# Optimization experiments

Measured on AMD Instinct MI355X. Metric: run time of the kernel, lower is better.

## Reference

```python
import jax, jax.numpy as jnp
import numpy as np

B, N, D, L = 8, 2048, 1024, 128


def setup_inputs() -> dict:
    key = jax.random.key(0)
    ks = jax.random.split(key, 8)
    return {
        "e_i_t_minus_1": jax.random.normal(ks[0], (B, D), dtype=jnp.float32),
        "e_j_t": jax.random.normal(ks[1], (B, N, D), dtype=jnp.float32),
        "imp_j_t": jax.random.uniform(ks[2], (B, N), dtype=jnp.float32),
        "R_lk": jax.random.normal(ks[3], (L, D), dtype=jnp.float32),
        "W_q": jax.random.normal(ks[4], (D, D), dtype=jnp.float32) * (D ** -0.5),
        "W_k": jax.random.normal(ks[5], (D, D), dtype=jnp.float32) * (D ** -0.5),
        "W_v": jax.random.normal(ks[6], (D, D), dtype=jnp.float32) * (D ** -0.5),
        "omega": jax.random.normal(ks[7], (D,), dtype=jnp.float32),
    }


def reference(e_i_t_minus_1, e_j_t, imp_j_t, R_lk, W_q, W_k, W_v, omega):
    # torch nn.Linear(x) = x @ W.T  (weights stored [out, in])
    q_i = jnp.einsum('bd,ed->be', e_i_t_minus_1, W_q)[:, None, :]   # [B,1,D]
    k_j = jnp.einsum('bnd,ed->bne', e_j_t, W_k)                      # [B,N,D]
    sigma = jnp.einsum('bnd,d->bn', jnp.tanh(q_i + k_j), omega)      # [B,N]
    exp_sigma = jnp.exp(sigma)
    sum_exp = jnp.sum(exp_sigma, axis=1, keepdims=True)              # [B,1]
    a_ij = imp_j_t * exp_sigma / (sum_exp + 1e-9)                    # [B,N]
    v_j = jnp.einsum('bnd,ed->bne', e_j_t, W_v)                      # [B,N,D]
    A = jnp.einsum('bn,bnd->bd', a_ij, v_j)                          # [B,D]
    # R_lk[l,d] * a_ij[b,n] * v_j[b,n,d], summed over n -> [B,L,D]
    A_lk = jnp.einsum('bn,bnd,ld->bld', a_ij, v_j, R_lk)             # [B,L,D]
    A_l = A                                                          # identical math in source
    return (A, A_lk, A_l)
```

## Files before the change

kernel.cpp:

```cpp
#include <hip/hip_runtime.h>
#include <hip/hip_bf16.h>
#include <math.h>

#define BB 8
#define NN 2048
#define DD 1024
#define LL 128
#define MM (BB*NN)

typedef _Float16 half8 __attribute__((ext_vector_type(8)));
typedef _Float16 half4 __attribute__((ext_vector_type(4)));
typedef __attribute__((ext_vector_type(4))) float floatx4;

__device__ __forceinline__ void glds16(const void* g, void* l) {
    __builtin_amdgcn_global_load_lds(
        (const __attribute__((address_space(1))) unsigned int*)g,
        (__attribute__((address_space(3))) unsigned int*)l, 16, 0, 0);
}

__global__ __launch_bounds__(256) void prep_kernel(const float* __restrict__ e_j,
                                                   _Float16* __restrict__ eh,
                                                   const float* __restrict__ Wk,
                                                   _Float16* __restrict__ wh,
                                                   const float* __restrict__ e_i,
                                                   const float* __restrict__ Wq,
                                                   float* __restrict__ q) {
    __shared__ float us[BB][DD];
    int blk = blockIdx.x;
    int tid = threadIdx.x;
    if (blk < 8192) {
        int i = blk * 256 + tid;
        const float4* xp = (const float4*)e_j + (size_t)i * 2;
        float4 v0 = xp[0], v1 = xp[1];
        half8 h;
        h[0] = (_Float16)v0.x; h[1] = (_Float16)v0.y;
        h[2] = (_Float16)v0.z; h[3] = (_Float16)v0.w;
        h[4] = (_Float16)v1.x; h[5] = (_Float16)v1.y;
        h[6] = (_Float16)v1.z; h[7] = (_Float16)v1.w;
        *(half8*)(eh + (size_t)i * 8) = h;
    } else if (blk < 8704) {
        int i = (blk - 8192) * 256 + tid;
        const float4* xp = (const float4*)Wk + (size_t)i * 2;
        float4 v0 = xp[0], v1 = xp[1];
        half8 h;
        h[0] = (_Float16)v0.x; h[1] = (_Float16)v0.y;
        h[2] = (_Float16)v0.z; h[3] = (_Float16)v0.w;
        h[4] = (_Float16)v1.x; h[5] = (_Float16)v1.y;
        h[6] = (_Float16)v1.z; h[7] = (_Float16)v1.w;
        *(half8*)(wh + (size_t)i * 8) = h;
    } else {
        for (int i = tid; i < BB * DD / 4; i += 256)
            ((float4*)&us[0][0])[i] = ((const float4*)e_i)[i];
        __syncthreads();
        int w = tid >> 6, lane = tid & 63;
        int d = (blk - 8704) * 4 + w;
        float acc[8] = {0.f, 0.f, 0.f, 0.f, 0.f, 0.f, 0.f, 0.f};
        for (int e0 = 0; e0 < DD; e0 += 256) {
            float4 wv = *(const float4*)&Wq[(size_t)d * DD + e0 + lane * 4];
            #pragma unroll
            for (int r = 0; r < 8; ++r) {
                float4 uv = *(const float4*)&us[r][e0 + lane * 4];
                acc[r] += wv.x * uv.x + wv.y * uv.y + wv.z * uv.z + wv.w * uv.w;
            }
        }
        #pragma unroll
        for (int r = 0; r < 8; ++r) {
            float s = acc[r];
            #pragma unroll
            for (int off = 32; off; off >>= 1) s += __shfl_down(s, off, 64);
            if (lane == 0) q[r * DD + d] = s;
        }
    }
}

__global__ __launch_bounds__(256) void sigma_mfma(const _Float16* __restrict__ eh,
                                                  const _Float16* __restrict__ wh,
                                                  const float* __restrict__ q,
                                                  const float* __restrict__ omega,
                                                  float* __restrict__ sig_part)
{
    __shared__ _Float16 Ah[128][32];
    __shared__ _Float16 Bh[128][32];
    __shared__ float red[128][2];

    const int tid  = threadIdx.x;
    const int lane = tid & 63;
    const int w    = tid >> 6;
    const int wr   = w >> 1, wc = w & 1;
    const int c15  = lane & 15, quad = lane >> 4;

    const int row0 = blockIdx.x * 128;
    const int col0 = blockIdx.y * 128;
    const int b    = row0 / NN;

    const int r0 = tid >> 2;
    const int ku = (tid & 3) * 8;

    const _Float16* gA = eh + (size_t)(row0 + r0) * DD + ku;
    const _Float16* gB = wh + (size_t)(col0 + r0) * DD + ku;

    char* dA = (char*)&Ah[0][0] + w * 1024;
    char* dB = (char*)&Bh[0][0] + w * 1024;

    floatx4 acc[4][4];
    #pragma unroll
    for (int i = 0; i < 4; ++i)
        #pragma unroll
        for (int j = 0; j < 4; ++j)
            acc[i][j] = (floatx4){0.f, 0.f, 0.f, 0.f};

    for (int k0 = 0; k0 < DD; k0 += 32) {
        glds16(gA + k0,                   dA);
        glds16(gA + (size_t)64 * DD + k0, dA + 4096);
        glds16(gB + k0,                   dB);
        glds16(gB + (size_t)64 * DD + k0, dB + 4096);
        __syncthreads();

        half8 a[4], bf[4];
        #pragma unroll
        for (int i = 0; i < 4; ++i) {
            a[i]  = *(const half8*)&Ah[wr * 64 + i * 16 + c15][quad * 8];
            bf[i] = *(const half8*)&Bh[wc * 64 + i * 16 + c15][quad * 8];
        }
        #pragma unroll
        for (int i = 0; i < 4; ++i)
            #pragma unroll
            for (int j = 0; j < 4; ++j)
                acc[i][j] = __builtin_amdgcn_mfma_f32_16x16x32_f16(a[i], bf[j], acc[i][j], 0, 0, 0);
        __syncthreads();
    }

    float part[4][4];
    #pragma unroll
    for (int i = 0; i < 4; ++i)
        #pragma unroll
        for (int r = 0; r < 4; ++r) part[i][r] = 0.f;

    #pragma unroll
    for (int j = 0; j < 4; ++j) {
        int c = col0 + wc * 64 + j * 16 + c15;
        float qv = q[b * DD + c];
        float om = omega[c];
        #pragma unroll
        for (int i = 0; i < 4; ++i)
            #pragma unroll
            for (int r = 0; r < 4; ++r)
                part[i][r] += tanhf(acc[i][j][r] + qv) * om;
    }
    #pragma unroll
    for (int i = 0; i < 4; ++i)
        #pragma unroll
        for (int r = 0; r < 4; ++r) {
            float s = part[i][r];
            s += __shfl_xor(s, 1, 64);
            s += __shfl_xor(s, 2, 64);
            s += __shfl_xor(s, 4, 64);
            s += __shfl_xor(s, 8, 64);
            if (c15 == 0) red[wr * 64 + i * 16 + quad * 4 + r][wc] = s;
        }
    __syncthreads();
    if (tid < 128)
        sig_part[blockIdx.y * MM + row0 + tid] = red[tid][0] + red[tid][1];
}

__global__ __launch_bounds__(256) void softmax_k(const float* __restrict__ sig_part,
                                                 const float* __restrict__ imp,
                                                 float* __restrict__ a_ij) {
    int b = blockIdx.x >> 3, slice = blockIdx.x & 7;
    int tid = threadIdx.x;
    __shared__ float red[256];
    float sv[8];
    float m = -1e30f;
    #pragma unroll
    for (int p = 0; p < 8; ++p) {
        int n = p * 256 + tid;
        float s = 0.f;
        #pragma unroll
        for (int db = 0; db < 8; ++db) s += sig_part[db * MM + b * NN + n];
        sv[p] = s;
        m = fmaxf(m, s);
    }
    red[tid] = m; __syncthreads();
    for (int off = 128; off; off >>= 1) {
        if (tid < off) red[tid] = fmaxf(red[tid], red[tid + off]);
        __syncthreads();
    }
    m = red[0]; __syncthreads();
    float sum = 0.f;
    #pragma unroll
    for (int p = 0; p < 8; ++p) sum += expf(sv[p] - m);
    red[tid] = sum; __syncthreads();
    for (int off = 128; off; off >>= 1) {
        if (tid < off) red[tid] += red[tid + off];
        __syncthreads();
    }
    float inv = 1.f / (red[0] + 1e-9f * expf(-m));
    int n = slice * 256 + tid;
    a_ij[b * NN + n] = imp[b * NN + n] * expf(sv[slice] - m) * inv;
}

__global__ __launch_bounds__(256) void u_kernel(const float* __restrict__ a_ij,
                                                const _Float16* __restrict__ eh,
                                                float* __restrict__ u_part) {
    int b = blockIdx.x >> 7, nc = blockIdx.x & 127;
    int t = threadIdx.x;
    float4 acc = {0.f, 0.f, 0.f, 0.f};
    const _Float16* base = eh + ((size_t)(b * NN + nc * 16)) * DD + t * 4;
    const float* ap = a_ij + b * NN + nc * 16;
    #pragma unroll
    for (int n = 0; n < 16; ++n) {
        float a = ap[n];
        half4 v = *(const half4*)(base + (size_t)n * DD);
        acc.x += a * (float)v[0]; acc.y += a * (float)v[1];
        acc.z += a * (float)v[2]; acc.w += a * (float)v[3];
    }
    *(float4*)(u_part + ((size_t)nc * BB + b) * DD + t * 4) = acc;
}

__global__ __launch_bounds__(256) void ureduce(const float* __restrict__ u_part,
                                               float* __restrict__ u) {
    int i = blockIdx.x * 256 + threadIdx.x;
    float s = 0.f;
    #pragma unroll 8
    for (int nc = 0; nc < 128; ++nc) s += u_part[(size_t)nc * BB * DD + i];
    u[i] = s;
}

__global__ __launch_bounds__(256) void rowdot8(const float* __restrict__ X,
                                               const float* __restrict__ W,
                                               float* __restrict__ out) {
    __shared__ float us[BB][DD];
    int tid = threadIdx.x;
    for (int i = tid; i < BB * DD / 4; i += 256)
        ((float4*)&us[0][0])[i] = ((const float4*)X)[i];
    __syncthreads();
    int w = tid >> 6, lane = tid & 63;
    int d = blockIdx.x * 4 + w;
    float acc[8] = {0.f, 0.f, 0.f, 0.f, 0.f, 0.f, 0.f, 0.f};
    for (int e0 = 0; e0 < DD; e0 += 256) {
        float4 wv = *(const float4*)&W[(size_t)d * DD + e0 + lane * 4];
        #pragma unroll
        for (int r = 0; r < 8; ++r) {
            float4 uv = *(const float4*)&us[r][e0 + lane * 4];
            acc[r] += wv.x * uv.x + wv.y * uv.y + wv.z * uv.z + wv.w * uv.w;
        }
    }
    #pragma unroll
    for (int r = 0; r < 8; ++r) {
        float s = acc[r];
        #pragma unroll
        for (int off = 32; off; off >>= 1) s += __shfl_down(s, off, 64);
        if (lane == 0) out[r * DD + d] = s;
    }
}

__global__ __launch_bounds__(256) void out_kernel(const float* __restrict__ A,
                                                  const float* __restrict__ Rlk,
                                                  float* __restrict__ out) {
    int i = blockIdx.x * 256 + threadIdx.x;
    int d = i & (DD - 1);
    int l = (i >> 10) & (LL - 1);
    int b = i >> 17;
    out[BB * DD + i] = A[b * DD + d] * Rlk[l * DD + d];
    if (i < BB * DD) {
        out[i] = A[i];
        out[BB * DD + BB * LL * DD + i] = A[i];
    }
}

extern "C" void kernel_launch(void* const* d_in, const int* in_sizes, int n_in,
                              void* d_out, int out_size, void* d_ws, size_t ws_size,
                              hipStream_t stream) {
    const float* e_i   = (const float*)d_in[0];
    const float* e_j   = (const float*)d_in[1];
    const float* imp   = (const float*)d_in[2];
    const float* Rlk   = (const float*)d_in[3];
    const float* Wq    = (const float*)d_in[4];
    const float* Wk    = (const float*)d_in[5];
    const float* Wv    = (const float*)d_in[6];
    const float* omega = (const float*)d_in[7];
    float* out = (float*)d_out;
    float* ws  = (float*)d_ws;

    float* q    = ws;
    float* sigp = ws + 8192;
    float* a_ij = ws + 139264;
    float* u    = ws + 155648;
    _Float16* eh = (_Float16*)(ws + 172032);
    _Float16* wh = eh + (size_t)MM * DD;
    float* u_part = (float*)(wh + (size_t)DD * DD);

    prep_kernel<<<8960, 256, 0, stream>>>(e_j, eh, Wk, wh, e_i, Wq, q);

    sigma_mfma<<<dim3(MM / 128, DD / 128), 256, 0, stream>>>(eh, wh, q, omega, sigp);

    softmax_k<<<64, 256, 0, stream>>>(sigp, imp, a_ij);

    u_kernel<<<1024, 256, 0, stream>>>(a_ij, eh, u_part);
    ureduce<<<32, 256, 0, stream>>>(u_part, u);

    rowdot8<<<256, 256, 0, stream>>>(u, Wv, a_ij);

    out_kernel<<<(BB * LL * DD) / 256, 256, 0, stream>>>(a_ij, Rlk, out);
}
```

Measured before the change: 209.8 us.

## Rewrite sigma GEMM with 256x256 tiles, 4-stage async LDS pipeline and swizzle

Replaces the 128x128 single-buffered sigma GEMM with a 256x256 tile kernel of 512 threads. It uses a 4-deep global_load_lds ring buffer with explicit vmcnt waits, an XOR-swizzled LDS layout to avoid bank conflicts, s_setprio around the MFMA bursts, and a remapped block order for L2 locality. The tanh epilogue switches to a fast exp/rcp approximation, and the column partials drop from 8 to 4, which softmax now sums. The aim is to hide global-load latency and raise MFMA utilisation, at the cost of more LDS (128KB), register pressure and a slightly less accurate tanh.

```diff
diff --git a/kernel.cpp b/kernel.cpp
--- a/kernel.cpp
+++ b/kernel.cpp
@@ -16,6 +16,14 @@
     __builtin_amdgcn_global_load_lds(
         (const __attribute__((address_space(1))) unsigned int*)g,
         (__attribute__((address_space(3))) unsigned int*)l, 16, 0, 0);
+}
+
+#define CFENCE() asm volatile("" ::: "memory")
+#define BARRIER() do { CFENCE(); __builtin_amdgcn_s_barrier(); CFENCE(); } while (0)
+
+__device__ __forceinline__ float ftanh(float x) {
+    float e = __expf(2.0f * x);
+    return 1.0f - 2.0f * __builtin_amdgcn_rcpf(e + 1.0f);
 }
 
 __global__ __launch_bounds__(256) void prep_kernel(const float* __restrict__ e_j,
@@ -73,94 +81,136 @@
     }
 }
 
-__global__ __launch_bounds__(256) void sigma_mfma(const _Float16* __restrict__ eh,
-                                                  const _Float16* __restrict__ wh,
-                                                  const float* __restrict__ q,
-                                                  const float* __restrict__ omega,
-                                                  float* __restrict__ sig_part)
+__global__ __launch_bounds__(512, 2) void sigma256(const _Float16* __restrict__ eh,
+                                                   const _Float16* __restrict__ wh,
+                                                   const float* __restrict__ q,
+                                                   const float* __restrict__ omega,
+                                                   float* __restrict__ sig_part)
 {
-    __shared__ _Float16 Ah[128][32];
-    __shared__ _Float16 Bh[128][32];
-    __shared__ float red[128][2];
+    __shared__ _Float16 As[4][256][32];
+    __shared__ _Float16 Bs[4][256][32];
 
     const int tid  = threadIdx.x;
     const int lane = tid & 63;
-    const int w    = tid >> 6;
-    const int wr   = w >> 1, wc = w & 1;
+    const int wid  = tid >> 6;
+    const int wr   = wid >> 2;
+    const int wc   = wid & 3;
     const int c15  = lane & 15, quad = lane >> 4;
 
-    const int row0 = blockIdx.x * 128;
-    const int col0 = blockIdx.y * 128;
-    const int b    = row0 / NN;
-
-    const int r0 = tid >> 2;
-    const int ku = (tid & 3) * 8;
-
-    const _Float16* gA = eh + (size_t)(row0 + r0) * DD + ku;
-    const _Float16* gB = wh + (size_t)(col0 + r0) * DD + ku;
-
-    char* dA = (char*)&Ah[0][0] + w * 1024;
-    char* dB = (char*)&Bh[0][0] + w * 1024;
-
-    floatx4 acc[4][4];
-    #pragma unroll
-    for (int i = 0; i < 4; ++i)
-        #pragma unroll
-        for (int j = 0; j < 4; ++j)
-            acc[i][j] = (floatx4){0.f, 0.f, 0.f, 0.f};
-
-    for (int k0 = 0; k0 < DD; k0 += 32) {
-        glds16(gA + k0,                   dA);
-        glds16(gA + (size_t)64 * DD + k0, dA + 4096);
-        glds16(gB + k0,                   dB);
-        glds16(gB + (size_t)64 * DD + k0, dB + 4096);
-        __syncthreads();
-
-        half8 a[4], bf[4];
-        #pragma unroll
-        for (int i = 0; i < 4; ++i) {
-            a[i]  = *(const half8*)&Ah[wr * 64 + i * 16 + c15][quad * 8];
-            bf[i] = *(const half8*)&Bh[wc * 64 + i * 16 + c15][quad * 8];
-        }
-        #pragma unroll
-        for (int i = 0; i < 4; ++i)
-            #pragma unroll
-            for (int j = 0; j < 4; ++j)
-                acc[i][j] = __builtin_amdgcn_mfma_f32_16x16x32_f16(a[i], bf[j], acc[i][j], 0, 0, 0);
-        __syncthreads();
-    }
-
-    float part[4][4];
-    #pragma unroll
-    for (int i = 0; i < 4; ++i)
-        #pragma unroll
-        for (int r = 0; r < 4; ++r) part[i][r] = 0.f;
-
-    #pragma unroll
-    for (int j = 0; j < 4; ++j) {
-        int c = col0 + wc * 64 + j * 16 + c15;
-        float qv = q[b * DD + c];
-        float om = omega[c];
-        #pragma unroll
-        for (int i = 0; i < 4; ++i)
+    const int wgid   = (blockIdx.x & 7) * 32 + (blockIdx.x >> 3);
+    const int colBlk = wgid >> 6;
+    const int rowBlk = wgid & 63;
+    const int row0   = rowBlk * 256;
+    const int col0   = colBlk * 256;
+    const int b      = row0 / NN;
+
+    const int srow = wid * 16 + (lane >> 2);
+    const int ssub = ((lane & 3) ^ ((lane >> 3) & 3)) * 8;
+    const _Float16* gA = eh + (size_t)(row0 + srow) * DD + ssub;
+    const _Float16* gB = wh + (size_t)(col0 + srow) * DD + ssub;
+    char* const ldsA0 = (char*)&As[0][0][0] + wid * 1024;
+    char* const ldsB0 = (char*)&Bs[0][0][0] + wid * 1024;
+
+#define STAGE_A(kt) do { int _bi = (kt) & 3; int _k0 = (kt) * 32;                  \
+        glds16(gA + _k0,                    ldsA0 + _bi * 16384);                  \
+        glds16(gA + (size_t)128 * DD + _k0, ldsA0 + _bi * 16384 + 8192); } while (0)
+#define STAGE_B(kt) do { int _bi = (kt) & 3; int _k0 = (kt) * 32;                  \
+        glds16(gB + _k0,                    ldsB0 + _bi * 16384);                  \
+        glds16(gB + (size_t)128 * DD + _k0, ldsB0 + _bi * 16384 + 8192); } while (0)
+
+    const char* const Abase = (const char*)&As[0][0][0];
+    const char* const Bbase = (const char*)&Bs[0][0][0];
+#define FRAG(base, bi, row, qd) \
+    (*(const half8*)((base) + (bi) * 16384 + (row) * 64 + ((((qd) ^ (((row) >> 1) & 3))) << 4)))
+
+    floatx4 acc[8][4];
+    #pragma unroll
+    for (int m = 0; m < 8; ++m)
+        #pragma unroll
+        for (int n = 0; n < 4; ++n) acc[m][n] = (floatx4){0.f, 0.f, 0.f, 0.f};
+
+    STAGE_A(0); STAGE_B(0);
+    STAGE_A(1); STAGE_B(1);
+    STAGE_A(2); STAGE_B(2);
+    asm volatile("s_waitcnt vmcnt(8)" ::: "memory");
+    BARRIER();
+
+#define TILE_BODY(t_, DO_STAGE, VMW)                                              \
+    {                                                                             \
+        const int bi = (t_) & 3;                                                  \
+        half8 a[4], bb[4];                                                        \
+        _Pragma("unroll")                                                         \
+        for (int m = 0; m < 4; ++m) a[m]  = FRAG(Abase, bi, wr * 128 + m * 16 + c15, quad); \
+        _Pragma("unroll")                                                         \
+        for (int n = 0; n < 4; ++n) bb[n] = FRAG(Bbase, bi, wc * 64  + n * 16 + c15, quad); \
+        if (DO_STAGE) STAGE_A((t_) + 3);                                          \
+        BARRIER();                                                                \
+        __builtin_amdgcn_s_setprio(1);                                            \
+        _Pragma("unroll")                                                         \
+        for (int m = 0; m < 4; ++m)                                               \
+            _Pragma("unroll")                                                     \
+            for (int n = 0; n < 4; ++n)                                           \
+                acc[m][n] = __builtin_amdgcn_mfma_f32_16x16x32_f16(a[m], bb[n], acc[m][n], 0, 0, 0); \
+        __builtin_amdgcn_s_setprio(0);                                            \
+        BARRIER();                                                                \
+        _Pragma("unroll")                                                         \
+        for (int m = 0; m < 4; ++m) a[m] = FRAG(Abase, bi, wr * 128 + 64 + m * 16 + c15, quad); \
+        if (DO_STAGE) STAGE_B((t_) + 3);                                          \
+        BARRIER();                                                                \
+        __builtin_amdgcn_s_setprio(1);                                            \
+        _Pragma("unroll")                                                         \
+        for (int m = 0; m < 4; ++m)                                               \
+            _Pragma("unroll")                                                     \
+            for (int n = 0; n < 4; ++n)                                           \
+                acc[4 + m][n] = __builtin_amdgcn_mfma_f32_16x16x32_f16(a[m], bb[n], acc[4 + m][n], 0, 0, 0); \
+        __builtin_amdgcn_s_setprio(0);                                            \
+        asm volatile("s_waitcnt vmcnt(" #VMW ")" ::: "memory");                   \
+        BARRIER();                                                                \
+    }
+
+    for (int t = 0; t < 29; ++t) TILE_BODY(t, 1, 8)
+    TILE_BODY(29, 0, 4)
+    TILE_BODY(30, 0, 0)
+    TILE_BODY(31, 0, 0)
+
+    float part[8][4];
+    #pragma unroll
+    for (int m = 0; m < 8; ++m)
+        #pragma unroll
+        for (int r = 0; r < 4; ++r) part[m][r] = 0.f;
+
+    #pragma unroll
+    for (int n = 0; n < 4; ++n) {
+        int col = col0 + wc * 64 + n * 16 + c15;
+        float qv = q[b * DD + col];
+        float om = omega[col];
+        #pragma unroll
+        for (int m = 0; m < 8; ++m)
             #pragma unroll
             for (int r = 0; r < 4; ++r)
-                part[i][r] += tanhf(acc[i][j][r] + qv) * om;
-    }
-    #pragma unroll
-    for (int i = 0; i < 4; ++i)
+                part[m][r] += ftanh(acc[m][n][r] + qv) * om;
+    }
+
+    float (*red)[4] = (float(*)[4])&As[0][0][0];
+    #pragma unroll
+    for (int m = 0; m < 8; ++m)
         #pragma unroll
         for (int r = 0; r < 4; ++r) {
-            float s = part[i][r];
+            float s = part[m][r];
             s += __shfl_xor(s, 1, 64);
             s += __shfl_xor(s, 2, 64);
             s += __shfl_xor(s, 4, 64);
             s += __shfl_xor(s, 8, 64);
-            if (c15 == 0) red[wr * 64 + i * 16 + quad * 4 + r][wc] = s;
+            if (c15 == 0) red[wr * 128 + m * 16 + quad * 4 + r][wc] = s;
         }
     __syncthreads();
-    if (tid < 128)
-        sig_part[blockIdx.y * MM + row0 + tid] = red[tid][0] + red[tid][1];
+    if (tid < 256)
+        sig_part[(size_t)colBlk * MM + row0 + tid] =
+            red[tid][0] + red[tid][1] + red[tid][2] + red[tid][3];
+#undef TILE_BODY
+#undef FRAG
+#undef STAGE_A
+#undef STAGE_B
 }
 
 __global__ __launch_bounds__(256) void softmax_k(const float* __restrict__ sig_part,
@@ -176,7 +226,7 @@
         int n = p * 256 + tid;
         float s = 0.f;
         #pragma unroll
-        for (int db = 0; db < 8; ++db) s += sig_part[db * MM + b * NN + n];
+        for (int db = 0; db < 4; ++db) s += sig_part[db * MM + b * NN + n];
         sv[p] = s;
         m = fmaxf(m, s);
     }
@@ -292,7 +342,7 @@
 
     prep_kernel<<<8960, 256, 0, stream>>>(e_j, eh, Wk, wh, e_i, Wq, q);
 
-    sigma_mfma<<<dim3(MM / 128, DD / 128), 256, 0, stream>>>(eh, wh, q, omega, sigp);
+    sigma256<<<dim3(256), 512, 0, stream>>>(eh, wh, q, omega, sigp);
 
     softmax_k<<<64, 256, 0, stream>>>(sigp, imp, a_ij);
 
```

Measured after the change: 189.8 us. 1.11x faster.
